# Kernel optimization log

Hardware: AMD Instinct MI355X
Metric: run time of the kernel (lower is better)

Reference implementation:

```python
import jax, jax.numpy as jnp
import numpy as np

N_SRC = 50000; N_DST = 50000; E = 800000
IN_NODE = 128; IN_EDGE = 16; OUT_NODE = 64; OUT_EDGE = 16; H = 4
LEAKY_SLOPE = 0.01  # F.leaky_relu default used inside dgl EGATConv


def setup_inputs() -> dict:
    key = jax.random.key(0)
    ks = jax.random.split(key, 11)
    return dict(
        nfeats=jax.random.normal(ks[0], (N_SRC, IN_NODE), jnp.float32),
        dst_feats=jax.random.normal(ks[1], (N_DST, IN_NODE), jnp.float32),
        reward=jax.random.uniform(ks[2], (E,), jnp.float32),
        src=jax.random.randint(ks[3], (E,), 0, N_SRC),
        dst=jax.random.randint(ks[4], (E,), 0, N_DST),
        W_ns=jax.random.normal(ks[5], (IN_NODE, H * OUT_NODE), jnp.float32) * 0.05,
        b_ns=jnp.zeros((H * OUT_NODE,), jnp.float32),
        W_ni=jax.random.normal(ks[6], (IN_NODE, H * OUT_EDGE), jnp.float32) * 0.05,
        W_nj=jax.random.normal(ks[7], (IN_NODE, H * OUT_EDGE), jnp.float32) * 0.05,
        W_fij=jax.random.normal(ks[8], (IN_EDGE, H * OUT_EDGE), jnp.float32) * 0.05,
        attn=jax.random.normal(ks[9], (H, OUT_EDGE), jnp.float32) * 0.05,
        b_e=jnp.zeros((H * OUT_EDGE,), jnp.float32),
    )


def reference(nfeats, dst_feats, reward, src, dst,
              W_ns, b_ns, W_ni, W_nj, W_fij, attn, b_e):
    # EGAT.forward with num_layers=1: efeats = reward repeated to IN_EDGE cols
    efeats = jnp.repeat(reward[:, None], IN_EDGE, axis=1)              # (E, Fe_in)
    # --- EGATConv ---
    f_ni = nfeats @ W_ni                                               # (Ns, H*Fe)
    f_nj = dst_feats @ W_nj                                            # (Nd, H*Fe)
    f_out = f_ni[src] + f_nj[dst] + efeats @ W_fij + b_e               # (E, H*Fe)
    f_out = jax.nn.leaky_relu(f_out, LEAKY_SLOPE).reshape(E, H, OUT_EDGE)
    e = jnp.einsum('ehf,hf->eh', f_out, attn)                          # (E, H)
    # edge softmax over incoming edges of each dst node (stable)
    m = jax.ops.segment_max(e, dst, num_segments=N_DST)                # (Nd, H)
    a = jnp.exp(e - m[dst])
    s = jax.ops.segment_sum(a, dst, num_segments=N_DST)                # (Nd, H)
    a = a / jnp.where(s > 0, s, 1.0)[dst]                              # (E, H)
    # weighted aggregation of projected src features
    h_src = (nfeats @ W_ns + b_ns).reshape(N_SRC, H, OUT_NODE)
    msg = h_src[src] * a[:, :, None]                                   # (E, H, Fn)
    h_out = jax.ops.segment_sum(msg, dst, num_segments=N_DST)          # (Nd, H, Fn)
    # wrapper: mean over heads then ReLU
    return jax.nn.relu(h_out.mean(axis=1))                             # (Nd, Fn)
```

## Files before the change

kernel.cpp:

```cpp
#include <hip/hip_runtime.h>

#define IN_NODE 128
#define OUT_NODE 64
#define NHEAD 4
#define HN 256
#define HE 64
#define LEAKY 0.01f

typedef __attribute__((ext_vector_type(8))) short bf16x8;
typedef __attribute__((ext_vector_type(4))) float f32x4;
typedef __attribute__((ext_vector_type(2))) float f32x2;

__device__ __forceinline__ float bf2f(unsigned short u) {
    union { unsigned u; float f; } v; v.u = ((unsigned)u) << 16; return v.f;
}
__device__ __forceinline__ unsigned short f2bf(float x) {
    union { float f; unsigned u; } v; v.f = x;
    unsigned r = v.u + 0x7FFF + ((v.u >> 16) & 1);
    return (unsigned short)(r >> 16);
}
__device__ __forceinline__ bf16x8 cvt8(float4 a, float4 b) {
    bf16x8 r;
    r[0] = (short)f2bf(a.x); r[1] = (short)f2bf(a.y);
    r[2] = (short)f2bf(a.z); r[3] = (short)f2bf(a.w);
    r[4] = (short)f2bf(b.x); r[5] = (short)f2bf(b.y);
    r[6] = (short)f2bf(b.z); r[7] = (short)f2bf(b.w);
    return r;
}
__device__ __forceinline__ f32x2 bfcvt2(unsigned d) {
    union { unsigned u; float f; } lo, hi;
    lo.u = d << 16; hi.u = d & 0xFFFF0000u;
    f32x2 r; r.x = lo.f; r.y = hi.f; return r;
}

__global__ void prep_w(const float* __restrict__ W_fij,
                       const float* __restrict__ W_ni,
                       const float* __restrict__ W_ns,
                       const float* __restrict__ W_nj,
                       float* __restrict__ wsum, unsigned short* __restrict__ WT) {
    int b = blockIdx.x;
    if (b == 0) {
        int k = threadIdx.x;
        if (k < 64) {
            float s = 0.f;
#pragma unroll
            for (int c = 0; c < 16; ++c) s += W_fij[c * 64 + k];
            wsum[k] = s;
        }
        return;
    }
    int base = (b - 1) * 4096 + threadIdx.x;
#pragma unroll
    for (int i = 0; i < 16; ++i) {
        int idx = base + i * 256;
        int g   = idx >> 11;
        int rem = idx & 2047;
        int c   = rem >> 9;
        int l   = (rem >> 3) & 63;
        int j   = rem & 7;
        int nl  = l & 15;
        int k   = c * 32 + (l >> 4) * 8 + j;
        unsigned short v;
        if (g < 4)       v = f2bf(W_ni[k * 64  + g * 16 + nl]);
        else if (g < 20) v = f2bf(W_ns[k * 256 + (g - 4) * 16 + nl]);
        else             v = f2bf(W_nj[k * 64  + (g - 20) * 16 + nl]);
        WT[idx] = v;
    }
}

__global__ __launch_bounds__(256) void scan_all(const int* __restrict__ cnt,
                                                int* __restrict__ row_ptr,
                                                int* __restrict__ partials,
                                                int* __restrict__ flags,
                                                int n, int E, int nb) {
    __shared__ int sums[256];
    __shared__ int s_base;
    int tid = threadIdx.x, b = blockIdx.x;
    int base = b * 1024;
    int v[4]; int tsum = 0;
#pragma unroll
    for (int j = 0; j < 4; ++j) {
        int idx = base + tid * 4 + j;
        v[j] = (idx < n) ? cnt[idx] : 0;
        tsum += v[j];
    }
    sums[tid] = tsum;
    __syncthreads();
    for (int off = 1; off < 256; off <<= 1) {
        int x = (tid >= off) ? sums[tid - off] : 0;
        __syncthreads();
        sums[tid] += x;
        __syncthreads();
    }
    if (tid == 255) {
        __hip_atomic_store(&partials[b], sums[255], __ATOMIC_RELAXED, __HIP_MEMORY_SCOPE_AGENT);
        __hip_atomic_store(&flags[b], 1, __ATOMIC_RELEASE, __HIP_MEMORY_SCOPE_AGENT);
    }
    if (tid < 64) {
        int val = 0;
        if (tid < nb) {
            while (__hip_atomic_load(&flags[tid], __ATOMIC_ACQUIRE, __HIP_MEMORY_SCOPE_AGENT) == 0) {
                __builtin_amdgcn_s_sleep(1);
            }
            val = __hip_atomic_load(&partials[tid], __ATOMIC_RELAXED, __HIP_MEMORY_SCOPE_AGENT);
        }
#pragma unroll
        for (int o = 1; o < 64; o <<= 1) {
            int x = __shfl_up(val, o);
            if (tid >= o) val += x;
        }
        int off = (b > 0) ? __shfl(val, b - 1) : 0;
        if (tid == 0) s_base = off;
    }
    __syncthreads();
    int run = s_base + sums[tid] - tsum;
#pragma unroll
    for (int j = 0; j < 4; ++j) {
        int idx = base + tid * 4 + j;
        if (idx < n) row_ptr[idx] = run;
        run += v[j];
    }
    if (b == nb - 1 && tid == 0) row_ptr[n] = E;
}

template<int NG, int G0>
__device__ __forceinline__ void gemm_tile(
    const float* __restrict__ A, int rowBase, int M,
    const unsigned short* __restrict__ WB, const float* __restrict__ b_ns,
    unsigned short* __restrict__ f_ni, unsigned short* __restrict__ h_src,
    unsigned short* __restrict__ f_nj, unsigned short* As)
{
    const int t = threadIdx.x;
    const float4* A4 = reinterpret_cast<const float4*>(A);
#pragma unroll
    for (int j = 0; j < 4; ++j) {
        int gi = j * 256 + t;
        int r  = gi >> 4;
        int gr = rowBase + r; if (gr >= M) gr = M - 1;
        int fi = (gi & 15) * 2;
        float4 a0 = A4[(size_t)gr * 32 + fi];
        float4 a1 = A4[(size_t)gr * 32 + fi + 1];
        int byteoff = (gi * 16) ^ ((r & 7) << 4);
        *reinterpret_cast<bf16x8*>(reinterpret_cast<char*>(As) + byteoff) = cvt8(a0, a1);
    }
    __syncthreads();

    const int lane = t & 63, w = t >> 6;
    const int rw = rowBase + w * 16;
    if (rw >= M) return;
    const int m = lane & 15, q = lane >> 4;
    const int tr = w * 16 + m;

    f32x4 acc[NG] = {};
    const char* Asb = reinterpret_cast<const char*>(As);
#pragma unroll
    for (int c = 0; c < 4; ++c) {
        int gi  = tr * 16 + c * 4 + q;
        int off = (gi * 16) ^ ((tr & 7) << 4);
        bf16x8 af = *reinterpret_cast<const bf16x8*>(Asb + off);
#pragma unroll
        for (int g = 0; g < NG; ++g) {
            bf16x8 bf = *reinterpret_cast<const bf16x8*>(
                WB + (size_t)(((G0 + g) * 4 + c) * 64 + lane) * 8);
            acc[g] = __builtin_amdgcn_mfma_f32_16x16x32_bf16(af, bf, acc[g], 0, 0, 0);
        }
    }

#pragma unroll
    for (int g = 0; g < NG; ++g) {
        const int ga = G0 + g;
        unsigned short* C; int N, colBase; const float* bias = nullptr;
        if (ga < 4)       { C = f_ni;  N = 64;  colBase = ga * 16; }
        else if (ga < 20) { C = h_src; N = 256; colBase = (ga - 4) * 16; bias = b_ns; }
        else              { C = f_nj;  N = 64;  colBase = (ga - 20) * 16; }
        int col = colBase + m;
        float bv = bias ? bias[col] : 0.f;
#pragma unroll
        for (int rr = 0; rr < 4; ++rr) {
            int orow = rw + q * 4 + rr;
            if (orow < M) C[(size_t)orow * N + col] = f2bf(acc[g][rr] + bv);
        }
    }
}

__device__ __forceinline__ void gemm_unit(
    int u, const float* __restrict__ nfeats, const float* __restrict__ dst_feats,
    const unsigned short* __restrict__ WT, const float* __restrict__ b_ns,
    unsigned short* __restrict__ f_ni, unsigned short* __restrict__ h_src,
    unsigned short* __restrict__ f_nj, unsigned short* As,
    int Ns, int Nd, int nBlkNf, int nBlkDj)
{
    if (u < 2 * nBlkNf) {
        int tile = u >> 1;
        if ((u & 1) == 0)
            gemm_tile<10, 0>(nfeats, tile * 64, Ns, WT, b_ns, f_ni, h_src, f_nj, As);
        else
            gemm_tile<10, 10>(nfeats, tile * 64, Ns, WT, b_ns, f_ni, h_src, f_nj, As);
    } else if (u < 2 * nBlkNf + nBlkDj) {
        gemm_tile<4, 20>(dst_feats, (u - 2 * nBlkNf) * 64, Nd, WT, b_ns, f_ni, h_src, f_nj, As);
    }
}

__global__ __launch_bounds__(256) void hist_gemm(
    const float* __restrict__ nfeats, const float* __restrict__ dst_feats,
    const unsigned short* __restrict__ WT, const float* __restrict__ b_ns,
    const int* __restrict__ dst,
    int* __restrict__ cnt, int* __restrict__ rank,
    unsigned short* __restrict__ f_ni, unsigned short* __restrict__ h_src,
    unsigned short* __restrict__ f_nj,
    int Ns, int Nd, int E, int nBlkNf, int nBlkDj, int u0, int u1)
{
    __shared__ __align__(16) unsigned short As[64 * 128];
    const int g = blockIdx.x >> 1, r = blockIdx.x & 1;
    if (r == 1) {
        int u = u0 + g;
        if (u < u1)
            gemm_unit(u, nfeats, dst_feats, WT, b_ns, f_ni, h_src, f_nj, As,
                      Ns, Nd, nBlkNf, nBlkDj);
        return;
    }
    int i = g * 256 + threadIdx.x;
    if (i < E) rank[i] = atomicAdd(&cnt[dst[i]], 1);
}

__global__ __launch_bounds__(256) void scat_gemm(
    const float* __restrict__ nfeats, const float* __restrict__ dst_feats,
    const unsigned short* __restrict__ WT, const float* __restrict__ b_ns,
    const int* __restrict__ src, const int* __restrict__ dst,
    const float* __restrict__ reward, const int* __restrict__ row_ptr,
    const int* __restrict__ rank, int2* __restrict__ sr_s,
    unsigned short* __restrict__ f_ni, unsigned short* __restrict__ h_src,
    unsigned short* __restrict__ f_nj,
    int Ns, int Nd, int E, int nBlkNf, int nBlkDj, int u0, int u1)
{
    __shared__ __align__(16) unsigned short As[64 * 128];
    const int g = blockIdx.x >> 1, r = blockIdx.x & 1;
    if (r == 1) {
        int u = u0 + g;
        if (u < u1)
            gemm_unit(u, nfeats, dst_feats, WT, b_ns, f_ni, h_src, f_nj, As,
                      Ns, Nd, nBlkNf, nBlkDj);
        return;
    }
    int i = g * 256 + threadIdx.x;
    if (i >= E) return;
    int d = dst[i];
    sr_s[row_ptr[d] + rank[i]] = make_int2(src[i], __float_as_int(reward[i]));
}

struct G { uint2 ui; uint4 h0; uint4 h1; };
__device__ __forceinline__ G gatherE(const unsigned short* __restrict__ f_ni,
                                     const unsigned short* __restrict__ h_src,
                                     int sn, int ll, int hq) {
    G g;
    g.ui = *reinterpret_cast<const uint2*>(f_ni + (size_t)sn * HE + 4 * ll);
    const unsigned short* hp = h_src + (size_t)sn * HN + hq;
    g.h0 = *reinterpret_cast<const uint4*>(hp);
    g.h1 = *reinterpret_cast<const uint4*>(hp + 8);
    return g;
}

__global__ __launch_bounds__(256) void fused_agg(
    const unsigned short* __restrict__ f_ni, const unsigned short* __restrict__ f_nj,
    const unsigned short* __restrict__ h_src, const int2* __restrict__ sr_s,
    const int* __restrict__ row_ptr,
    const float* __restrict__ wsum, const float* __restrict__ b_e,
    const float* __restrict__ attn, float* __restrict__ out, int Nd)
{
    __shared__ float red[4][1024];
    const int wv = threadIdx.x >> 6, lane = threadIdx.x & 63;
    const int d = blockIdx.x * 4 + wv;
    if (d >= Nd) return;
    const int ll = lane & 15, sub = lane >> 4;
    const int hq = ((lane >> 2) & 3) * 64 + (lane & 3) * 16;
    const int mql = (lane >> 1) & 3;

    float4 wsv = *reinterpret_cast<const float4*>(wsum + 4 * ll);
    float4 bev = *reinterpret_cast<const float4*>(b_e + 4 * ll);
    float4 atv = *reinterpret_cast<const float4*>(attn + 4 * ll);
    f32x2 ws01 = {wsv.x, wsv.y}, ws23 = {wsv.z, wsv.w};
    f32x2 at01 = {atv.x, atv.y}, at23 = {atv.z, atv.w};
    const f32x2 lk2 = {LEAKY, LEAKY};

    const int beg = row_ptr[d];
    const int end = row_ptr[d + 1];
    const int deg = end - beg;

    float den = 0.f;
    f32x2 a0 = {}, a1 = {}, a2 = {}, a3 = {}, a4 = {}, a5 = {}, a6 = {}, a7 = {};

    if (deg > 0) {
        uint2 uj = *reinterpret_cast<const uint2*>(f_nj + (size_t)d * HE + 4 * ll);
        f32x2 bb01 = bfcvt2(uj.x) + (f32x2){bev.x, bev.y};
        f32x2 bb23 = bfcvt2(uj.y) + (f32x2){bev.z, bev.w};
        const int nq = (deg + 3) >> 2;
        const int last = end - 1;

#define LDSR(q) ({ int qq_ = ((q) < nq) ? (q) : (nq - 1);                 \
                   int slot_ = beg + qq_ * 4 + sub;                       \
                   if (slot_ > last) slot_ = last;                        \
                   sr_s[slot_]; })

#define COMPUTE(sr, gg, kq) do {                                          \
    float r_ = __int_as_float((sr).y);                                    \
    f32x2 r2_ = {r_, r_};                                                 \
    f32x2 v01_ = bfcvt2((gg).ui.x) + r2_ * ws01 + bb01;                   \
    f32x2 v23_ = bfcvt2((gg).ui.y) + r2_ * ws23 + bb23;                   \
    v01_ = __builtin_elementwise_max(v01_, v01_ * lk2);                   \
    v23_ = __builtin_elementwise_max(v23_, v23_ * lk2);                   \
    f32x2 t2_ = v01_ * at01 + v23_ * at23;                                \
    float t_ = t2_.x + t2_.y;                                             \
    t_ += __shfl_xor(t_, 1);                                              \
    t_ += __shfl_xor(t_, 2);                                              \
    float ev_ = ((beg + (kq) * 4 + sub) < end) ? __expf(t_) : 0.f;        \
    den += ev_;                                                           \
    f32x2 ev2_ = {ev_, ev_};                                              \
    a0 += bfcvt2((gg).h0.x) * ev2_;                                       \
    a1 += bfcvt2((gg).h0.y) * ev2_;                                       \
    a2 += bfcvt2((gg).h0.z) * ev2_;                                       \
    a3 += bfcvt2((gg).h0.w) * ev2_;                                       \
    a4 += bfcvt2((gg).h1.x) * ev2_;                                       \
    a5 += bfcvt2((gg).h1.y) * ev2_;                                       \
    a6 += bfcvt2((gg).h1.z) * ev2_;                                       \
    a7 += bfcvt2((gg).h1.w) * ev2_;                                       \
} while (0)

        int2 sr0 = LDSR(0), sr1 = LDSR(1);
        G gA = gatherE(f_ni, h_src, sr0.x, ll, hq);
        for (int k = 0; k < nq; ++k) {
            int2 sr2 = LDSR(k + 2);
            G gB = gatherE(f_ni, h_src, sr1.x, ll, hq);
            COMPUTE(sr0, gA, k);
            sr0 = sr1; sr1 = sr2; gA = gB;
        }
#undef COMPUTE
#undef LDSR
    }

    den += __shfl_xor(den, 16);
    den += __shfl_xor(den, 32);
    float sc = (den > 0.f) ? 0.25f / den : 0.f;
    float* wr = &red[wv][lane * 16];
    float4 s0 = {a0.x * sc, a0.y * sc, a1.x * sc, a1.y * sc};
    float4 s1 = {a2.x * sc, a2.y * sc, a3.x * sc, a3.y * sc};
    float4 s2 = {a4.x * sc, a4.y * sc, a5.x * sc, a5.y * sc};
    float4 s3 = {a6.x * sc, a6.y * sc, a7.x * sc, a7.y * sc};
    *reinterpret_cast<float4*>(wr + ((0 ^ mql) << 2)) = s0;
    *reinterpret_cast<float4*>(wr + ((1 ^ mql) << 2)) = s1;
    *reinterpret_cast<float4*>(wr + ((2 ^ mql) << 2)) = s2;
    *reinterpret_cast<float4*>(wr + ((3 ^ mql) << 2)) = s3;
    asm volatile("s_waitcnt lgkmcnt(0)" ::: "memory");
    float ssum = 0.f;
    const int e = lane & 15, c45 = lane >> 4;
#pragma unroll
    for (int s = 0; s < 4; ++s)
#pragma unroll
        for (int h = 0; h < 4; ++h) {
            int L = s * 16 + h * 4 + c45;
            int m2 = (L >> 1) & 3;
            int fi = L * 16 + (((e >> 2) ^ m2) << 2) + (e & 3);
            ssum += red[wv][fi];
        }
    out[(size_t)d * OUT_NODE + lane] = fmaxf(ssum, 0.f);
}

static inline char* align256(char* p) {
    return (char*)(((uintptr_t)p + 255) & ~(uintptr_t)255);
}

extern "C" void kernel_launch(void* const* d_in, const int* in_sizes, int n_in,
                              void* d_out, int out_size, void* d_ws, size_t ws_size,
                              hipStream_t stream) {
    const float* nfeats    = (const float*)d_in[0];
    const float* dst_feats = (const float*)d_in[1];
    const float* reward    = (const float*)d_in[2];
    const int*   src       = (const int*)d_in[3];
    const int*   dst       = (const int*)d_in[4];
    const float* W_ns      = (const float*)d_in[5];
    const float* b_ns      = (const float*)d_in[6];
    const float* W_ni      = (const float*)d_in[7];
    const float* W_nj      = (const float*)d_in[8];
    const float* W_fij     = (const float*)d_in[9];
    const float* attn      = (const float*)d_in[10];
    const float* b_e       = (const float*)d_in[11];
    float* out = (float*)d_out;

    const int Ns = in_sizes[0] / IN_NODE;
    const int Nd = in_sizes[1] / IN_NODE;
    const int E  = in_sizes[2];

    char* ws = (char*)d_ws;
    unsigned short* f_ni  = (unsigned short*)ws; ws = align256(ws + (size_t)Ns * HE * 2);
    unsigned short* f_nj  = (unsigned short*)ws; ws = align256(ws + (size_t)Nd * HE * 2);
    unsigned short* h_src = (unsigned short*)ws; ws = align256(ws + (size_t)Ns * HN * 2);
    unsigned short* WT    = (unsigned short*)ws; ws = align256(ws + 49152 * 2);
    float* wsum    = (float*)ws; ws = align256(ws + HE * 4);
    int*   cnt     = (int*)ws;
    int*   flags   = cnt + Nd;   ws = align256(ws + (size_t)(Nd + 64) * 4);
    int*   row_ptr = (int*)ws;   ws = align256(ws + (size_t)(Nd + 1) * 4);
    int*   partials= (int*)ws;   ws = align256(ws + 256 * 4);
    int2*  sr_s    = (int2*)ws;  ws = align256(ws + (size_t)E * 8);
    int*   rank    = (int*)ws;   ws = align256(ws + (size_t)E * 4);

    hipMemsetAsync(cnt, 0, (size_t)(Nd + 64) * 4, stream);

    prep_w<<<13, 256, 0, stream>>>(W_fij, W_ni, W_ns, W_nj, wsum, WT);

    int nBlkNf = (Ns + 63) / 64;
    int nBlkDj = (Nd + 63) / 64;
    int nU  = 2 * nBlkNf + nBlkDj;
    int nUA = (nU + 1) / 2;
    int nE256 = (E + 255) / 256;

    int g1 = (nE256 > nUA) ? nE256 : nUA;
    hist_gemm<<<g1 * 2, 256, 0, stream>>>(
        nfeats, dst_feats, WT, b_ns, dst, cnt, rank,
        f_ni, h_src, f_nj, Ns, Nd, E, nBlkNf, nBlkDj, 0, nUA);

    int nb = (Nd + 1023) / 1024;
    scan_all<<<nb, 256, 0, stream>>>(cnt, row_ptr, partials, flags, Nd, E, nb);

    int nUB = nU - nUA;
    int g3 = (nE256 > nUB) ? nE256 : nUB;
    scat_gemm<<<g3 * 2, 256, 0, stream>>>(
        nfeats, dst_feats, WT, b_ns, src, dst, reward, row_ptr, rank, sr_s,
        f_ni, h_src, f_nj, Ns, Nd, E, nBlkNf, nBlkDj, nUA, nU);

    fused_agg<<<(Nd + 3) / 4, 256, 0, stream>>>(
        f_ni, f_nj, h_src, sr_s, row_ptr, wsum, b_e, attn, out, Nd);
}
```

Measured before the change: 253.1 us.

## Overlap scan with GEMM tiles and fold count zeroing into weight prep

Replaces the hipMemsetAsync of the count buffer with extra blocks in the weight-prep kernel, which removes one stream operation. The standalone scan kernel becomes scan_gemm, which co-schedules the prefix scan with a slice of the GEMM tiles so the tiny scan launch is not left running alone on the device. GEMM work is repartitioned across the three phases (46%/8%/rest). The scan's spin-wait on flags now shares the grid with GEMM blocks, so there is some risk to forward progress or added latency if scan blocks are not all resident at once.

```diff
diff --git a/kernel.cpp b/kernel.cpp
--- a/kernel.cpp
+++ b/kernel.cpp
@@ -33,11 +33,12 @@
     f32x2 r; r.x = lo.f; r.y = hi.f; return r;
 }
 
-__global__ void prep_w(const float* __restrict__ W_fij,
+__global__ void prep_z(const float* __restrict__ W_fij,
                        const float* __restrict__ W_ni,
                        const float* __restrict__ W_ns,
                        const float* __restrict__ W_nj,
-                       float* __restrict__ wsum, unsigned short* __restrict__ WT) {
+                       float* __restrict__ wsum, unsigned short* __restrict__ WT,
+                       int* __restrict__ cnt, int nZero) {
     int b = blockIdx.x;
     if (b == 0) {
         int k = threadIdx.x;
@@ -49,78 +50,30 @@
         }
         return;
     }
-    int base = (b - 1) * 4096 + threadIdx.x;
-#pragma unroll
-    for (int i = 0; i < 16; ++i) {
-        int idx = base + i * 256;
-        int g   = idx >> 11;
-        int rem = idx & 2047;
-        int c   = rem >> 9;
-        int l   = (rem >> 3) & 63;
-        int j   = rem & 7;
-        int nl  = l & 15;
-        int k   = c * 32 + (l >> 4) * 8 + j;
-        unsigned short v;
-        if (g < 4)       v = f2bf(W_ni[k * 64  + g * 16 + nl]);
-        else if (g < 20) v = f2bf(W_ns[k * 256 + (g - 4) * 16 + nl]);
-        else             v = f2bf(W_nj[k * 64  + (g - 20) * 16 + nl]);
-        WT[idx] = v;
-    }
-}
-
-__global__ __launch_bounds__(256) void scan_all(const int* __restrict__ cnt,
-                                                int* __restrict__ row_ptr,
-                                                int* __restrict__ partials,
-                                                int* __restrict__ flags,
-                                                int n, int E, int nb) {
-    __shared__ int sums[256];
-    __shared__ int s_base;
-    int tid = threadIdx.x, b = blockIdx.x;
-    int base = b * 1024;
-    int v[4]; int tsum = 0;
-#pragma unroll
-    for (int j = 0; j < 4; ++j) {
-        int idx = base + tid * 4 + j;
-        v[j] = (idx < n) ? cnt[idx] : 0;
-        tsum += v[j];
-    }
-    sums[tid] = tsum;
-    __syncthreads();
-    for (int off = 1; off < 256; off <<= 1) {
-        int x = (tid >= off) ? sums[tid - off] : 0;
-        __syncthreads();
-        sums[tid] += x;
-        __syncthreads();
-    }
-    if (tid == 255) {
-        __hip_atomic_store(&partials[b], sums[255], __ATOMIC_RELAXED, __HIP_MEMORY_SCOPE_AGENT);
-        __hip_atomic_store(&flags[b], 1, __ATOMIC_RELEASE, __HIP_MEMORY_SCOPE_AGENT);
-    }
-    if (tid < 64) {
-        int val = 0;
-        if (tid < nb) {
-            while (__hip_atomic_load(&flags[tid], __ATOMIC_ACQUIRE, __HIP_MEMORY_SCOPE_AGENT) == 0) {
-                __builtin_amdgcn_s_sleep(1);
-            }
-            val = __hip_atomic_load(&partials[tid], __ATOMIC_RELAXED, __HIP_MEMORY_SCOPE_AGENT);
-        }
-#pragma unroll
-        for (int o = 1; o < 64; o <<= 1) {
-            int x = __shfl_up(val, o);
-            if (tid >= o) val += x;
-        }
-        int off = (b > 0) ? __shfl(val, b - 1) : 0;
-        if (tid == 0) s_base = off;
-    }
-    __syncthreads();
-    int run = s_base + sums[tid] - tsum;
-#pragma unroll
-    for (int j = 0; j < 4; ++j) {
-        int idx = base + tid * 4 + j;
-        if (idx < n) row_ptr[idx] = run;
-        run += v[j];
-    }
-    if (b == nb - 1 && tid == 0) row_ptr[n] = E;
+    if (b <= 12) {
+        int base = (b - 1) * 4096 + threadIdx.x;
+#pragma unroll
+        for (int i = 0; i < 16; ++i) {
+            int idx = base + i * 256;
+            int g   = idx >> 11;
+            int rem = idx & 2047;
+            int c   = rem >> 9;
+            int l   = (rem >> 3) & 63;
+            int j   = rem & 7;
+            int nl  = l & 15;
+            int k   = c * 32 + (l >> 4) * 8 + j;
+            unsigned short v;
+            if (g < 4)       v = f2bf(W_ni[k * 64  + g * 16 + nl]);
+            else if (g < 20) v = f2bf(W_ns[k * 256 + (g - 4) * 16 + nl]);
+            else             v = f2bf(W_nj[k * 64  + (g - 20) * 16 + nl]);
+            WT[idx] = v;
+        }
+        return;
+    }
+    int base = (b - 13) * 1024 + threadIdx.x * 4;
+#pragma unroll
+    for (int j = 0; j < 4; ++j)
+        if (base + j < nZero) cnt[base + j] = 0;
 }
 
 template<int NG, int G0>
@@ -221,6 +174,77 @@
     }
     int i = g * 256 + threadIdx.x;
     if (i < E) rank[i] = atomicAdd(&cnt[dst[i]], 1);
+}
+
+__global__ __launch_bounds__(256) void scan_gemm(
+    const int* __restrict__ cnt, int* __restrict__ row_ptr,
+    int* __restrict__ partials, int* __restrict__ flags,
+    int n, int E, int nb,
+    const float* __restrict__ nfeats, const float* __restrict__ dst_feats,
+    const unsigned short* __restrict__ WT, const float* __restrict__ b_ns,
+    unsigned short* __restrict__ f_ni, unsigned short* __restrict__ h_src,
+    unsigned short* __restrict__ f_nj,
+    int Ns, int Nd, int nBlkNf, int nBlkDj, int u0, int u1)
+{
+    __shared__ __align__(16) unsigned short As[64 * 128];
+    __shared__ int sums[256];
+    __shared__ int s_base;
+    const int g = blockIdx.x >> 1, r = blockIdx.x & 1;
+    if (r == 1) {
+        int u = u0 + g;
+        if (u < u1)
+            gemm_unit(u, nfeats, dst_feats, WT, b_ns, f_ni, h_src, f_nj, As,
+                      Ns, Nd, nBlkNf, nBlkDj);
+        return;
+    }
+    const int b = g;
+    if (b >= nb) return;
+    int tid = threadIdx.x;
+    int base = b * 1024;
+    int v[4]; int tsum = 0;
+#pragma unroll
+    for (int j = 0; j < 4; ++j) {
+        int idx = base + tid * 4 + j;
+        v[j] = (idx < n) ? cnt[idx] : 0;
+        tsum += v[j];
+    }
+    sums[tid] = tsum;
+    __syncthreads();
+    for (int off = 1; off < 256; off <<= 1) {
+        int x = (tid >= off) ? sums[tid - off] : 0;
+        __syncthreads();
+        sums[tid] += x;
+        __syncthreads();
+    }
+    if (tid == 255) {
+        __hip_atomic_store(&partials[b], sums[255], __ATOMIC_RELAXED, __HIP_MEMORY_SCOPE_AGENT);
+        __hip_atomic_store(&flags[b], 1, __ATOMIC_RELEASE, __HIP_MEMORY_SCOPE_AGENT);
+    }
+    if (tid < 64) {
+        int val = 0;
+        if (tid < nb) {
+            while (__hip_atomic_load(&flags[tid], __ATOMIC_ACQUIRE, __HIP_MEMORY_SCOPE_AGENT) == 0) {
+                __builtin_amdgcn_s_sleep(1);
+            }
+            val = __hip_atomic_load(&partials[tid], __ATOMIC_RELAXED, __HIP_MEMORY_SCOPE_AGENT);
+        }
+#pragma unroll
+        for (int o = 1; o < 64; o <<= 1) {
+            int x = __shfl_up(val, o);
+            if (tid >= o) val += x;
+        }
+        int off = (b > 0) ? __shfl(val, b - 1) : 0;
+        if (tid == 0) s_base = off;
+    }
+    __syncthreads();
+    int run = s_base + sums[tid] - tsum;
+#pragma unroll
+    for (int j = 0; j < 4; ++j) {
+        int idx = base + tid * 4 + j;
+        if (idx < n) row_ptr[idx] = run;
+        run += v[j];
+    }
+    if (b == nb - 1 && tid == 0) row_ptr[n] = E;
 }
 
 __global__ __launch_bounds__(256) void scat_gemm(
@@ -402,29 +426,35 @@
     int2*  sr_s    = (int2*)ws;  ws = align256(ws + (size_t)E * 8);
     int*   rank    = (int*)ws;   ws = align256(ws + (size_t)E * 4);
 
-    hipMemsetAsync(cnt, 0, (size_t)(Nd + 64) * 4, stream);
-
-    prep_w<<<13, 256, 0, stream>>>(W_fij, W_ni, W_ns, W_nj, wsum, WT);
+    const int nZero = Nd + 64;
+    int nZblk = (nZero + 1023) / 1024;
+    prep_z<<<13 + nZblk, 256, 0, stream>>>(
+        W_fij, W_ni, W_ns, W_nj, wsum, WT, cnt, nZero);
 
     int nBlkNf = (Ns + 63) / 64;
     int nBlkDj = (Nd + 63) / 64;
     int nU  = 2 * nBlkNf + nBlkDj;
-    int nUA = (nU + 1) / 2;
+    int uA  = (int)((long long)nU * 46 / 100);
+    int uS  = (int)((long long)nU * 8 / 100);
     int nE256 = (E + 255) / 256;
-
-    int g1 = (nE256 > nUA) ? nE256 : nUA;
+    int nb = (Nd + 1023) / 1024;
+
+    int g1 = (nE256 > uA) ? nE256 : uA;
     hist_gemm<<<g1 * 2, 256, 0, stream>>>(
         nfeats, dst_feats, WT, b_ns, dst, cnt, rank,
-        f_ni, h_src, f_nj, Ns, Nd, E, nBlkNf, nBlkDj, 0, nUA);
-
-    int nb = (Nd + 1023) / 1024;
-    scan_all<<<nb, 256, 0, stream>>>(cnt, row_ptr, partials, flags, Nd, E, nb);
-
-    int nUB = nU - nUA;
+        f_ni, h_src, f_nj, Ns, Nd, E, nBlkNf, nBlkDj, 0, uA);
+
+    int g2 = (nb > uS) ? nb : uS;
+    scan_gemm<<<g2 * 2, 256, 0, stream>>>(
+        cnt, row_ptr, partials, flags, Nd, E, nb,
+        nfeats, dst_feats, WT, b_ns, f_ni, h_src, f_nj,
+        Ns, Nd, nBlkNf, nBlkDj, uA, uA + uS);
+
+    int uB0 = uA + uS, nUB = nU - uB0;
     int g3 = (nE256 > nUB) ? nE256 : nUB;
     scat_gemm<<<g3 * 2, 256, 0, stream>>>(
         nfeats, dst_feats, WT, b_ns, src, dst, reward, row_ptr, rank, sr_s,
-        f_ni, h_src, f_nj, Ns, Nd, E, nBlkNf, nBlkDj, nUA, nU);
+        f_ni, h_src, f_nj, Ns, Nd, E, nBlkNf, nBlkDj, uB0, nU);
 
     fused_agg<<<(Nd + 3) / 4, 256, 0, stream>>>(
         f_ni, f_nj, h_src, sr_s, row_ptr, wsum, b_e, attn, out, Nd);
```

Result: no change. 252.5 us (-0.2%).
